# Optimization experiments

Measured on AMD Instinct MI355X. Metric: run time of the kernel, lower is better.

The kernel has to match this reference:

```python
import jax, jax.numpy as jnp
import numpy as np

NUM_THRESHOLDS = 200
N = 4_000_000
KEPS = 1e-07
EPS = 1e-06


def _make_thresholds(num_thresholds=NUM_THRESHOLDS):
    inner = [(i + 1) * 1.0 / (num_thresholds - 1) for i in range(num_thresholds - 2)]
    return jnp.asarray([0.0 - KEPS] + inner + [1.0 + KEPS], dtype=jnp.float32)


def setup_inputs() -> dict:
    key = jax.random.key(0)
    k1, k2 = jax.random.split(key)
    predictions = jax.random.uniform(k1, (N,), dtype=jnp.float32)  # in [0,1]
    labels = jax.random.randint(k2, (N,), 0, 2, dtype=jnp.int32)
    thresholds = _make_thresholds()
    return {"predictions": predictions, "labels": labels, "thresholds": thresholds}


def reference(predictions, labels, thresholds):
    # Confusion matrix at all thresholds: [T, N] broadcast compare, reduce over N.
    lab_pos = labels.astype(bool)  # [N]
    pred_pos = predictions[None, :] > thresholds[:, None]  # [T, N] bool
    lab_pos_b = jnp.broadcast_to(lab_pos[None, :], pred_pos.shape)
    tp = jnp.sum(jnp.logical_and(lab_pos_b, pred_pos), axis=1).astype(jnp.float32)
    fn = jnp.sum(jnp.logical_and(lab_pos_b, ~pred_pos), axis=1).astype(jnp.float32)
    fp = jnp.sum(jnp.logical_and(~lab_pos_b, pred_pos), axis=1).astype(jnp.float32)
    tn = jnp.sum(jnp.logical_and(~lab_pos_b, ~pred_pos), axis=1).astype(jnp.float32)
    # Trapezoidal AUC over (FPR, TPR)
    rec = (tp + EPS) / (tp + fn + EPS)          # y (TPR)
    fp_rate = fp / (fp + tn + EPS)              # x (FPR)
    x, y = fp_rate, rec
    auc = jnp.sum((x[:-1] - x[1:]) * (y[:-1] + y[1:]) * 0.5)
    return auc
```

## Files before the change

kernel.cpp:

```cpp
#include <hip/hip_runtime.h>

#define NTH    200
#define NBINS  201
#define NBLKH  1024
#define HTPB   256
#define HWAVES 4

__global__ void __launch_bounds__(HTPB)
auroc_hist_kernel(const float* __restrict__ preds,
                  const int*   __restrict__ labels,
                  const float* __restrict__ thresholds,
                  unsigned int* __restrict__ part,
                  int n) {
    __shared__ float        s_th[NTH];
    __shared__ unsigned int s_hist[HWAVES][NBINS];

    const int t    = threadIdx.x;
    const int wave = t >> 6;

    for (int i = t; i < NTH; i += HTPB)
        s_th[i] = thresholds[i];
    for (int i = t; i < HWAVES * NBINS; i += HTPB)
        ((unsigned int*)s_hist)[i] = 0u;
    __syncthreads();

    unsigned int* my = s_hist[wave];

    const int gid = blockIdx.x * HTPB + t;
    const int S   = gridDim.x * HTPB;
    const int n4  = n >> 2;
    const float4* p4 = (const float4*)preds;
    const int4*   l4 = (const int4*)labels;

    int i = gid;
    for (; i + S < n4; i += 2 * S) {
        float4 pa = p4[i];
        int4   la = l4[i];
        float4 pb = p4[i + S];
        int4   lb = l4[i + S];

        float pv[8] = {pa.x, pa.y, pa.z, pa.w, pb.x, pb.y, pb.z, pb.w};
        int   lv[8] = {la.x, la.y, la.z, la.w, lb.x, lb.y, lb.z, lb.w};
#pragma unroll
        for (int j = 0; j < 8; ++j) {
            float pp = pv[j];
            int k0 = (int)(pp * 199.0f);
            k0 = k0 > 198 ? 198 : k0;
            float ta = s_th[k0];
            float tb = s_th[k0 + 1];
            int g = k0 + (ta < pp) + (tb < pp);
            unsigned int add = 1u | ((unsigned int)lv[j] << 16);
            atomicAdd(&my[g], add);
        }
    }
    for (; i < n4; i += S) {
        float4 p = p4[i];
        int4   l = l4[i];
        float pv[4] = {p.x, p.y, p.z, p.w};
        int   lv[4] = {l.x, l.y, l.z, l.w};
#pragma unroll
        for (int j = 0; j < 4; ++j) {
            float pp = pv[j];
            int k0 = (int)(pp * 199.0f);
            k0 = k0 > 198 ? 198 : k0;
            float ta = s_th[k0];
            float tb = s_th[k0 + 1];
            int g = k0 + (ta < pp) + (tb < pp);
            unsigned int add = 1u | ((unsigned int)lv[j] << 16);
            atomicAdd(&my[g], add);
        }
    }
    for (int k = (n4 << 2) + gid; k < n; k += S) {
        float pp = preds[k];
        int k0 = (int)(pp * 199.0f);
        k0 = k0 > 198 ? 198 : k0;
        float ta = s_th[k0];
        float tb = s_th[k0 + 1];
        int g = k0 + (ta < pp) + (tb < pp);
        unsigned int add = 1u | ((unsigned int)labels[k] << 16);
        atomicAdd(&my[g], add);
    }
    __syncthreads();

    const int b = blockIdx.x;
    for (int i2 = t; i2 < NBINS; i2 += HTPB) {
        unsigned int v = s_hist[0][i2] + s_hist[1][i2] + s_hist[2][i2] + s_hist[3][i2];
        unsigned int pos = v >> 16;
        unsigned int neg = (v & 0xFFFFu) - pos;
        part[i2 * NBLKH + b] = (pos << 16) | neg;
    }
}

__global__ void __launch_bounds__(256)
auroc_reduce_kernel(const unsigned int* __restrict__ part,
                    unsigned int* __restrict__ g_pos,
                    unsigned int* __restrict__ g_neg) {
    __shared__ unsigned int s_w[HWAVES][2];

    const int t = threadIdx.x;
    const int r = blockIdx.x;

    uint4 v = ((const uint4*)(part + r * NBLKH))[t];
    unsigned int ap = (v.x >> 16) + (v.y >> 16) + (v.z >> 16) + (v.w >> 16);
    unsigned int an = (v.x & 0xFFFFu) + (v.y & 0xFFFFu) +
                      (v.z & 0xFFFFu) + (v.w & 0xFFFFu);
#pragma unroll
    for (int off = 32; off >= 1; off >>= 1) {
        ap += __shfl_down(ap, off, 64);
        an += __shfl_down(an, off, 64);
    }
    if ((t & 63) == 0) { s_w[t >> 6][0] = ap; s_w[t >> 6][1] = an; }
    __syncthreads();

    if (t == 0) {
        g_pos[r] = s_w[0][0] + s_w[1][0] + s_w[2][0] + s_w[3][0];
        g_neg[r] = s_w[0][1] + s_w[1][1] + s_w[2][1] + s_w[3][1];
    }
}

__global__ void __launch_bounds__(256)
auroc_finish_kernel(const unsigned int* __restrict__ g_pos,
                    const unsigned int* __restrict__ g_neg,
                    float* __restrict__ out) {
    __shared__ unsigned int s_pos[NBINS], s_neg[NBINS];
    __shared__ unsigned int s_sufp[NBINS + 1], s_sufn[NBINS + 1];
    __shared__ float s_x[NTH], s_y[NTH];

    const int t = threadIdx.x;

    if (t < NBINS) { s_pos[t] = g_pos[t]; s_neg[t] = g_neg[t]; }
    if (t == 0)    { s_sufp[NBINS] = 0u; s_sufn[NBINS] = 0u; }
    __syncthreads();

    if (t < NBINS) {
        unsigned int sp = 0u, sn = 0u;
        for (int k = t; k < NBINS; ++k) { sp += s_pos[k]; sn += s_neg[k]; }
        s_sufp[t] = sp;
        s_sufn[t] = sn;
    }
    __syncthreads();

    const float P   = (float)s_sufp[0];
    const float Nn  = (float)s_sufn[0];
    const float EPS = 1e-6f;

    if (t < NTH) {
        float tp = (float)s_sufp[t + 1];
        float fp = (float)s_sufn[t + 1];
        float fn = P - tp;
        float tn = Nn - fp;
        s_y[t] = (tp + EPS) / (tp + fn + EPS);
        s_x[t] = fp / (fp + tn + EPS);
    }
    __syncthreads();

    if (t == 0) {
        double auc = 0.0;
        for (int i = 0; i < NTH - 1; ++i)
            auc += (double)((s_x[i] - s_x[i + 1]) * (s_y[i] + s_y[i + 1]) * 0.5f);
        out[0] = (float)auc;
    }
}

extern "C" void kernel_launch(void* const* d_in, const int* in_sizes, int n_in,
                              void* d_out, int out_size, void* d_ws, size_t ws_size,
                              hipStream_t stream) {
    const float* preds      = (const float*)d_in[0];
    const int*   labels     = (const int*)d_in[1];
    const float* thresholds = (const float*)d_in[2];
    float*       out        = (float*)d_out;
    unsigned int* part      = (unsigned int*)d_ws;
    unsigned int* g_pos     = part + NBINS * NBLKH;
    unsigned int* g_neg     = g_pos + NBINS;

    const int n = in_sizes[0];

    auroc_hist_kernel<<<NBLKH, HTPB, 0, stream>>>(preds, labels, thresholds,
                                                  part, n);
    auroc_reduce_kernel<<<NBINS, 256, 0, stream>>>(part, g_pos, g_neg);
    auroc_finish_kernel<<<1, 256, 0, stream>>>(g_pos, g_neg, out);
}
```

Before: 87.56 us.

## Fuse histogram, reduce and finish into one cooperative kernel with grid sync

```diff
diff --git a/kernel.cpp b/kernel.cpp
--- a/kernel.cpp
+++ b/kernel.cpp
@@ -1,33 +1,40 @@
 #include <hip/hip_runtime.h>
+#include <hip/hip_cooperative_groups.h>
+
+namespace cg = cooperative_groups;
 
 #define NTH    200
 #define NBINS  201
-#define NBLKH  1024
-#define HTPB   256
-#define HWAVES 4
+#define NBLK   256
+#define TPB    1024
+#define NWAVES 16
 
-__global__ void __launch_bounds__(HTPB)
-auroc_hist_kernel(const float* __restrict__ preds,
-                  const int*   __restrict__ labels,
-                  const float* __restrict__ thresholds,
-                  unsigned int* __restrict__ part,
-                  int n) {
+__global__ void __launch_bounds__(TPB, 4)
+auroc_fused(const float* __restrict__ preds,
+            const int*   __restrict__ labels,
+            const float* __restrict__ thresholds,
+            unsigned int* __restrict__ part,
+            float* __restrict__ out,
+            int n) {
     __shared__ float        s_th[NTH];
-    __shared__ unsigned int s_hist[HWAVES][NBINS];
+    __shared__ unsigned int s_hist[NWAVES][NBINS];
+    __shared__ unsigned int s_rp[NBINS], s_rn[NBINS];
+    __shared__ unsigned int s_sufp[NBINS + 1], s_sufn[NBINS + 1];
+    __shared__ float        s_x[NTH], s_y[NTH];
 
     const int t    = threadIdx.x;
     const int wave = t >> 6;
 
-    for (int i = t; i < NTH; i += HTPB)
+    for (int i = t; i < NTH; i += TPB)
         s_th[i] = thresholds[i];
-    for (int i = t; i < HWAVES * NBINS; i += HTPB)
+    for (int i = t; i < NWAVES * NBINS; i += TPB)
         ((unsigned int*)s_hist)[i] = 0u;
     __syncthreads();
 
     unsigned int* my = s_hist[wave];
 
-    const int gid = blockIdx.x * HTPB + t;
-    const int S   = gridDim.x * HTPB;
+    const int gid = blockIdx.x * TPB + t;
+    const int S   = NBLK * TPB;
     const int n4  = n >> 2;
     const float4* p4 = (const float4*)preds;
     const int4*   l4 = (const int4*)labels;
@@ -83,81 +90,62 @@
     __syncthreads();
 
     const int b = blockIdx.x;
-    for (int i2 = t; i2 < NBINS; i2 += HTPB) {
-        unsigned int v = s_hist[0][i2] + s_hist[1][i2] + s_hist[2][i2] + s_hist[3][i2];
+    for (int i2 = t; i2 < NBINS; i2 += TPB) {
+        unsigned int v = 0u;
+#pragma unroll
+        for (int w = 0; w < NWAVES; ++w) v += s_hist[w][i2];
         unsigned int pos = v >> 16;
         unsigned int neg = (v & 0xFFFFu) - pos;
-        part[i2 * NBLKH + b] = (pos << 16) | neg;
+        part[i2 * NBLK + b] = (pos << 16) | neg;
     }
-}
 
-__global__ void __launch_bounds__(256)
-auroc_reduce_kernel(const unsigned int* __restrict__ part,
-                    unsigned int* __restrict__ g_pos,
-                    unsigned int* __restrict__ g_neg) {
-    __shared__ unsigned int s_w[HWAVES][2];
+    __threadfence();
+    cg::this_grid().sync();
 
-    const int t = threadIdx.x;
-    const int r = blockIdx.x;
+    if (blockIdx.x != 0) return;
 
-    uint4 v = ((const uint4*)(part + r * NBLKH))[t];
-    unsigned int ap = (v.x >> 16) + (v.y >> 16) + (v.z >> 16) + (v.w >> 16);
-    unsigned int an = (v.x & 0xFFFFu) + (v.y & 0xFFFFu) +
-                      (v.z & 0xFFFFu) + (v.w & 0xFFFFu);
+    const int lane = t & 63;
+    for (int r = wave; r < NBINS; r += NWAVES) {
+        uint4 v = ((const uint4*)(part + r * NBLK))[lane];
+        unsigned int ap = (v.x >> 16) + (v.y >> 16) + (v.z >> 16) + (v.w >> 16);
+        unsigned int an = (v.x & 0xFFFFu) + (v.y & 0xFFFFu) +
+                          (v.z & 0xFFFFu) + (v.w & 0xFFFFu);
 #pragma unroll
-    for (int off = 32; off >= 1; off >>= 1) {
-        ap += __shfl_down(ap, off, 64);
-        an += __shfl_down(an, off, 64);
+        for (int off = 32; off >= 1; off >>= 1) {
+            ap += __shfl_down(ap, off, 64);
+            an += __shfl_down(an, off, 64);
+        }
+        if (lane == 0) { s_rp[r] = ap; s_rn[r] = an; }
     }
-    if ((t & 63) == 0) { s_w[t >> 6][0] = ap; s_w[t >> 6][1] = an; }
     __syncthreads();
 
-    if (t == 0) {
-        g_pos[r] = s_w[0][0] + s_w[1][0] + s_w[2][0] + s_w[3][0];
-        g_neg[r] = s_w[0][1] + s_w[1][1] + s_w[2][1] + s_w[3][1];
-    }
-}
-
-__global__ void __launch_bounds__(256)
-auroc_finish_kernel(const unsigned int* __restrict__ g_pos,
-                    const unsigned int* __restrict__ g_neg,
-                    float* __restrict__ out) {
-    __shared__ unsigned int s_pos[NBINS], s_neg[NBINS];
-    __shared__ unsigned int s_sufp[NBINS + 1], s_sufn[NBINS + 1];
-    __shared__ float s_x[NTH], s_y[NTH];
-
-    const int t = threadIdx.x;
-
-    if (t < NBINS) { s_pos[t] = g_pos[t]; s_neg[t] = g_neg[t]; }
-    if (t == 0)    { s_sufp[NBINS] = 0u; s_sufn[NBINS] = 0u; }
-    __syncthreads();
-
+    if (t == 0) { s_sufp[NBINS] = 0u; s_sufn[NBINS] = 0u; }
     if (t < NBINS) {
         unsigned int sp = 0u, sn = 0u;
-        for (int k = t; k < NBINS; ++k) { sp += s_pos[k]; sn += s_neg[k]; }
+        for (int k = t; k < NBINS; ++k) { sp += s_rp[k]; sn += s_rn[k]; }
         s_sufp[t] = sp;
         s_sufn[t] = sn;
     }
     __syncthreads();
 
-    const float P   = (float)s_sufp[0];
-    const float Nn  = (float)s_sufn[0];
-    const float EPS = 1e-6f;
+    const float P    = (float)s_sufp[0];
+    const float Nn   = (float)s_sufn[0];
+    const float EPSf = 1e-6f;
 
     if (t < NTH) {
         float tp = (float)s_sufp[t + 1];
         float fp = (float)s_sufn[t + 1];
         float fn = P - tp;
         float tn = Nn - fp;
-        s_y[t] = (tp + EPS) / (tp + fn + EPS);
-        s_x[t] = fp / (fp + tn + EPS);
+        s_y[t] = (tp + EPSf) / (tp + fn + EPSf);
+        s_x[t] = fp / (fp + tn + EPSf);
     }
     __syncthreads();
 
     if (t == 0) {
         double auc = 0.0;
-        for (int i = 0; i < NTH - 1; ++i)
-            auc += (double)((s_x[i] - s_x[i + 1]) * (s_y[i] + s_y[i + 1]) * 0.5f);
+        for (int q = 0; q < NTH - 1; ++q)
+            auc += (double)((s_x[q] - s_x[q + 1]) * (s_y[q] + s_y[q + 1]) * 0.5f);
         out[0] = (float)auc;
     }
 }
@@ -170,13 +158,10 @@
     const float* thresholds = (const float*)d_in[2];
     float*       out        = (float*)d_out;
     unsigned int* part      = (unsigned int*)d_ws;
-    unsigned int* g_pos     = part + NBINS * NBLKH;
-    unsigned int* g_neg     = g_pos + NBINS;
+    int n = in_sizes[0];
 
-    const int n = in_sizes[0];
-
-    auroc_hist_kernel<<<NBLKH, HTPB, 0, stream>>>(preds, labels, thresholds,
-                                                  part, n);
-    auroc_reduce_kernel<<<NBINS, 256, 0, stream>>>(part, g_pos, g_neg);
-    auroc_finish_kernel<<<1, 256, 0, stream>>>(g_pos, g_neg, out);
+    void* args[] = {(void*)&preds, (void*)&labels, (void*)&thresholds,
+                    (void*)&part, (void*)&out, (void*)&n};
+    hipLaunchCooperativeKernel(reinterpret_cast<void*>(auroc_fused),
+                               dim3(NBLK), dim3(TPB), args, 0, stream);
 }
```

New measurement: 201.7 us. +130.3%, slower.

## Merge reduce and finish kernels; halve histogram grid; parallelize AUC sum

Applied to the files above, without the earlier changes.

```diff
diff --git a/kernel.cpp b/kernel.cpp
--- a/kernel.cpp
+++ b/kernel.cpp
@@ -2,7 +2,7 @@
 
 #define NTH    200
 #define NBINS  201
-#define NBLKH  1024
+#define NBLKH  512
 #define HTPB   256
 #define HWAVES 4
 
@@ -27,7 +27,7 @@
     unsigned int* my = s_hist[wave];
 
     const int gid = blockIdx.x * HTPB + t;
-    const int S   = gridDim.x * HTPB;
+    const int S   = NBLKH * HTPB;
     const int n4  = n >> 2;
     const float4* p4 = (const float4*)preds;
     const int4*   l4 = (const int4*)labels;
@@ -91,74 +91,68 @@
     }
 }
 
-__global__ void __launch_bounds__(256)
-auroc_reduce_kernel(const unsigned int* __restrict__ part,
-                    unsigned int* __restrict__ g_pos,
-                    unsigned int* __restrict__ g_neg) {
-    __shared__ unsigned int s_w[HWAVES][2];
+__global__ void __launch_bounds__(1024)
+auroc_finish_kernel(const unsigned int* __restrict__ part,
+                    float* __restrict__ out) {
+    __shared__ unsigned int s_rp[NBINS], s_rn[NBINS];
+    __shared__ unsigned int s_sufp[NBINS + 1], s_sufn[NBINS + 1];
+    __shared__ float s_x[NTH], s_y[NTH], s_term[NTH];
 
-    const int t = threadIdx.x;
-    const int r = blockIdx.x;
+    const int t    = threadIdx.x;
+    const int wave = t >> 6;
+    const int lane = t & 63;
 
-    uint4 v = ((const uint4*)(part + r * NBLKH))[t];
-    unsigned int ap = (v.x >> 16) + (v.y >> 16) + (v.z >> 16) + (v.w >> 16);
-    unsigned int an = (v.x & 0xFFFFu) + (v.y & 0xFFFFu) +
-                      (v.z & 0xFFFFu) + (v.w & 0xFFFFu);
+    for (int r = wave; r < NBINS; r += 16) {
+        const uint4* row4 = (const uint4*)(part + r * NBLKH);
+        uint4 a = row4[lane];
+        uint4 b = row4[lane + 64];
+        unsigned int ap = (a.x >> 16) + (a.y >> 16) + (a.z >> 16) + (a.w >> 16)
+                        + (b.x >> 16) + (b.y >> 16) + (b.z >> 16) + (b.w >> 16);
+        unsigned int an = (a.x & 0xFFFFu) + (a.y & 0xFFFFu) + (a.z & 0xFFFFu) + (a.w & 0xFFFFu)
+                        + (b.x & 0xFFFFu) + (b.y & 0xFFFFu) + (b.z & 0xFFFFu) + (b.w & 0xFFFFu);
 #pragma unroll
-    for (int off = 32; off >= 1; off >>= 1) {
-        ap += __shfl_down(ap, off, 64);
-        an += __shfl_down(an, off, 64);
+        for (int off = 32; off >= 1; off >>= 1) {
+            ap += __shfl_down(ap, off, 64);
+            an += __shfl_down(an, off, 64);
+        }
+        if (lane == 0) { s_rp[r] = ap; s_rn[r] = an; }
     }
-    if ((t & 63) == 0) { s_w[t >> 6][0] = ap; s_w[t >> 6][1] = an; }
     __syncthreads();
 
-    if (t == 0) {
-        g_pos[r] = s_w[0][0] + s_w[1][0] + s_w[2][0] + s_w[3][0];
-        g_neg[r] = s_w[0][1] + s_w[1][1] + s_w[2][1] + s_w[3][1];
-    }
-}
-
-__global__ void __launch_bounds__(256)
-auroc_finish_kernel(const unsigned int* __restrict__ g_pos,
-                    const unsigned int* __restrict__ g_neg,
-                    float* __restrict__ out) {
-    __shared__ unsigned int s_pos[NBINS], s_neg[NBINS];
-    __shared__ unsigned int s_sufp[NBINS + 1], s_sufn[NBINS + 1];
-    __shared__ float s_x[NTH], s_y[NTH];
-
-    const int t = threadIdx.x;
-
-    if (t < NBINS) { s_pos[t] = g_pos[t]; s_neg[t] = g_neg[t]; }
-    if (t == 0)    { s_sufp[NBINS] = 0u; s_sufn[NBINS] = 0u; }
-    __syncthreads();
-
+    if (t == 0) { s_sufp[NBINS] = 0u; s_sufn[NBINS] = 0u; }
     if (t < NBINS) {
         unsigned int sp = 0u, sn = 0u;
-        for (int k = t; k < NBINS; ++k) { sp += s_pos[k]; sn += s_neg[k]; }
+        for (int k = t; k < NBINS; ++k) { sp += s_rp[k]; sn += s_rn[k]; }
         s_sufp[t] = sp;
         s_sufn[t] = sn;
     }
     __syncthreads();
 
-    const float P   = (float)s_sufp[0];
-    const float Nn  = (float)s_sufn[0];
-    const float EPS = 1e-6f;
+    const float P    = (float)s_sufp[0];
+    const float Nn   = (float)s_sufn[0];
+    const float EPSf = 1e-6f;
 
     if (t < NTH) {
         float tp = (float)s_sufp[t + 1];
         float fp = (float)s_sufn[t + 1];
         float fn = P - tp;
         float tn = Nn - fp;
-        s_y[t] = (tp + EPS) / (tp + fn + EPS);
-        s_x[t] = fp / (fp + tn + EPS);
+        s_y[t] = (tp + EPSf) / (tp + fn + EPSf);
+        s_x[t] = fp / (fp + tn + EPSf);
     }
     __syncthreads();
 
-    if (t == 0) {
-        double auc = 0.0;
-        for (int i = 0; i < NTH - 1; ++i)
-            auc += (double)((s_x[i] - s_x[i + 1]) * (s_y[i] + s_y[i + 1]) * 0.5f);
-        out[0] = (float)auc;
+    if (t < NTH - 1)
+        s_term[t] = (s_x[t] - s_x[t + 1]) * (s_y[t] + s_y[t + 1]) * 0.5f;
+    __syncthreads();
+
+    if (t < 64) {
+        double s = 0.0;
+        for (int q = t; q < NTH - 1; q += 64) s += (double)s_term[q];
+#pragma unroll
+        for (int off = 32; off >= 1; off >>= 1)
+            s += __shfl_down(s, off, 64);
+        if (t == 0) out[0] = (float)s;
     }
 }
 
@@ -170,13 +164,9 @@
     const float* thresholds = (const float*)d_in[2];
     float*       out        = (float*)d_out;
     unsigned int* part      = (unsigned int*)d_ws;
-    unsigned int* g_pos     = part + NBINS * NBLKH;
-    unsigned int* g_neg     = g_pos + NBINS;
-
     const int n = in_sizes[0];
 
     auroc_hist_kernel<<<NBLKH, HTPB, 0, stream>>>(preds, labels, thresholds,
                                                   part, n);
-    auroc_reduce_kernel<<<NBINS, 256, 0, stream>>>(part, g_pos, g_neg);
-    auroc_finish_kernel<<<1, 256, 0, stream>>>(g_pos, g_neg, out);
+    auroc_finish_kernel<<<1, 1024, 0, stream>>>(part, out);
 }
```

Measured after the change: 88.94 us. No clear change (+1.6%).
